# Performance work log

Hardware: AMD Instinct MI355X
Metric: run time of the kernel (lower is better)

Reference implementation:

```python
import jax, jax.numpy as jnp
import numpy as np

B, N, D, H = 4, 1024, 1024, 16
DH = D // H
SCALE = jnp.sqrt(jnp.float32(DH))


def setup_inputs() -> dict:
    key = jax.random.key(0)
    ks = jax.random.split(key, 12)
    Q = jax.random.normal(ks[0], (B, N, D), dtype=jnp.float32)
    K = jax.random.normal(ks[1], (B, N, D), dtype=jnp.float32)
    V = jax.random.normal(ks[2], (B, N, D), dtype=jnp.float32)
    mask = jax.random.bernoulli(ks[3], 0.1, (B, H, N, N))
    w_scale = 0.02
    Wq = jax.random.normal(ks[4], (D, D), dtype=jnp.float32) * w_scale
    Wk = jax.random.normal(ks[5], (D, D), dtype=jnp.float32) * w_scale
    Wv = jax.random.normal(ks[6], (D, D), dtype=jnp.float32) * w_scale
    Wo = jax.random.normal(ks[7], (D, D), dtype=jnp.float32) * w_scale
    bq = jax.random.normal(ks[8], (D,), dtype=jnp.float32) * w_scale
    bk = jax.random.normal(ks[9], (D,), dtype=jnp.float32) * w_scale
    bv = jax.random.normal(ks[10], (D,), dtype=jnp.float32) * w_scale
    bo = jax.random.normal(ks[11], (D,), dtype=jnp.float32) * w_scale
    return {"Q": Q, "K": K, "V": V, "mask": mask,
            "Wq": Wq, "bq": bq, "Wk": Wk, "bk": bk,
            "Wv": Wv, "bv": bv, "Wo": Wo, "bo": bo}


def _split_heads(x):
    # [b, n, (h d)] -> [b, h, n, d]
    b, n, _ = x.shape
    return x.reshape(b, n, H, DH).transpose(0, 2, 1, 3)


def reference(Q, K, V, mask, Wq, bq, Wk, bk, Wv, bv, Wo, bo):
    # torch nn.Linear: y = x @ W.T + b
    q = _split_heads(Q @ Wq.T + bq)
    k = _split_heads(K @ Wk.T + bk)
    v = _split_heads(V @ Wv.T + bv)
    # scores: [b, h, n, n]
    scores = jnp.einsum('bhnd,bhmd->bhnm', q, k) / SCALE
    scores = jnp.where(mask, jnp.float32(-1e10), scores)
    weights = jax.nn.softmax(scores, axis=-1)
    attn = jnp.einsum('bhnm,bhmd->bhnd', weights, v)
    x = attn.transpose(0, 2, 1, 3).reshape(Q.shape[0], Q.shape[1], D)
    x = x @ Wo.T + bo
    return (x, weights)
```

## Files before the change

### kernel.cpp

```cpp
#include <hip/hip_runtime.h>


#define SEQ   1024
#define D_DIM 1024
#define HEADS 16
#define DHEAD 64
#define BATCH 4

typedef __attribute__((ext_vector_type(8))) short bhalf8;
typedef __attribute__((ext_vector_type(4))) float floatx4;

typedef __attribute__((address_space(1))) const void GlobCV;
typedef __attribute__((address_space(3))) void LdsV;

static __device__ __forceinline__ unsigned short f2b(float f) {
    unsigned int u = __float_as_uint(f);
    u += 0x7FFFu + ((u >> 16) & 1u);
    return (unsigned short)(u >> 16);
}

static __device__ __forceinline__ void gload16(const void* g, void* l) {
    __builtin_amdgcn_global_load_lds((GlobCV*)g, (LdsV*)l, 16, 0, 0);
}

__global__ __launch_bounds__(256) void detect_mask_kernel(const uint4* __restrict__ m,
                                                          int* __restrict__ flag) {
    __shared__ int found;
    if (threadIdx.x == 0) found = 0;
    __syncthreads();
    unsigned int bad = 0;
#pragma unroll
    for (int i = 0; i < 16; ++i) {
        uint4 w = m[threadIdx.x + i * 256];
        unsigned int a = w.x, b = w.y, c = w.z, d = w.w;
        bad |= (a != 0u && a != 1u && a != 0x3F800000u);
        bad |= (b != 0u && b != 1u && b != 0x3F800000u);
        bad |= (c != 0u && c != 1u && c != 0x3F800000u);
        bad |= (d != 0u && d != 1u && d != 0x3F800000u);
    }
    if (bad) atomicOr(&found, 1);
    __syncthreads();
    if (threadIdx.x == 0) *flag = found;
}

__global__ __launch_bounds__(256) void mask_pack(const void* __restrict__ mask,
                                                 const int* __restrict__ mflagp,
                                                 unsigned int* __restrict__ bits) {
    const size_t idx = (size_t)blockIdx.x * 256 + threadIdx.x;
    unsigned int w = 0;
    if (*mflagp) {
        const uint4* p = (const uint4*)mask + idx * 2;
        uint4 a = p[0], b = p[1];
        unsigned int d[8] = {a.x, a.y, a.z, a.w, b.x, b.y, b.z, b.w};
#pragma unroll
        for (int i = 0; i < 8; ++i) {
            unsigned int x = d[i];
            w |= (((x & 0x000000FFu) != 0u) ? 1u : 0u) << (i * 4 + 0);
            w |= (((x & 0x0000FF00u) != 0u) ? 1u : 0u) << (i * 4 + 1);
            w |= (((x & 0x00FF0000u) != 0u) ? 1u : 0u) << (i * 4 + 2);
            w |= (((x & 0xFF000000u) != 0u) ? 1u : 0u) << (i * 4 + 3);
        }
    } else {
        const uint4* p = (const uint4*)mask + idx * 8;
#pragma unroll
        for (int i = 0; i < 8; ++i) {
            uint4 a = p[i];
            w |= (a.x ? 1u : 0u) << (i * 4 + 0);
            w |= (a.y ? 1u : 0u) << (i * 4 + 1);
            w |= (a.z ? 1u : 0u) << (i * 4 + 2);
            w |= (a.w ? 1u : 0u) << (i * 4 + 3);
        }
    }
    bits[idx] = w;
}

__global__ __launch_bounds__(256) void cast_f2b_all(const float* __restrict__ Q,
                                                    const float* __restrict__ K,
                                                    const float* __restrict__ V,
                                                    const float* __restrict__ Wq,
                                                    const float* __restrict__ Wk,
                                                    const float* __restrict__ Wv,
                                                    const float* __restrict__ Wo,
                                                    unsigned short* __restrict__ Ab,
                                                    unsigned short* __restrict__ Wb) {
    const int y = blockIdx.y;
    const float* src;
    unsigned short* dst;
    int nblocks;
    if (y < 3) {
        src = (y == 0) ? Q : (y == 1) ? K : V;
        dst = Ab + ((size_t)y << 22);
        nblocks = 2048;
    } else {
        src = (y == 3) ? Wq : (y == 4) ? Wk : (y == 5) ? Wv : Wo;
        dst = Wb + ((size_t)(y - 3) << 20);
        nblocks = 512;
    }
    if (blockIdx.x >= (unsigned)nblocks) return;
    const size_t i = ((size_t)blockIdx.x * 256 + threadIdx.x) * 8;
    float4 f0 = *(const float4*)&src[i];
    float4 f1 = *(const float4*)&src[i + 4];
    ushort4 h0, h1;
    h0.x = f2b(f0.x); h0.y = f2b(f0.y); h0.z = f2b(f0.z); h0.w = f2b(f0.w);
    h1.x = f2b(f1.x); h1.y = f2b(f1.y); h1.z = f2b(f1.z); h1.w = f2b(f1.w);
    *(ushort4*)&dst[i] = h0;
    *(ushort4*)&dst[i + 4] = h1;
}

template <int OMODE>
__global__ __launch_bounds__(256) void gemm_lds(const unsigned short* __restrict__ Abase,
                                                const unsigned short* __restrict__ Wbase,
                                                const float* __restrict__ b0,
                                                const float* __restrict__ b1,
                                                const float* __restrict__ b2,
                                                void* __restrict__ Obase) {
    __shared__ unsigned short Al[128 * 64];
    __shared__ unsigned short Bl[128 * 64];

    const int tid = threadIdx.x;
    const int lane = tid & 63, wid = tid >> 6;
    const int lr = lane & 15, lq = lane >> 4;
    const int wm = (wid & 1) * 64, wn = (wid >> 1) * 64;
    const int rowBase = blockIdx.y * 128;
    const int colBase = blockIdx.x * 128;
    const int z = blockIdx.z;

    const unsigned short* A = Abase + ((size_t)z << 22);
    const unsigned short* W = Wbase + ((size_t)z << 20);
    const float* bias = (z == 0) ? b0 : (z == 1) ? b1 : b2;

    const int srow = lane >> 3;
    const int scol = (lane & 7) * 8;

    floatx4 acc[4][4];
#pragma unroll
    for (int mi = 0; mi < 4; ++mi)
#pragma unroll
        for (int ni = 0; ni < 4; ++ni)
#pragma unroll
            for (int r = 0; r < 4; ++r) acc[mi][ni][r] = 0.f;

    for (int k0 = 0; k0 < D_DIM; k0 += 64) {
#pragma unroll
        for (int i = 0; i < 4; ++i) {
            int chunk = wid * 4 + i;
            gload16(&A[(size_t)(rowBase + chunk * 8 + srow) * D_DIM + k0 + scol],
                    &Al[chunk * 512]);
        }
#pragma unroll
        for (int i = 0; i < 4; ++i) {
            int chunk = wid * 4 + i;
            gload16(&W[(size_t)(colBase + chunk * 8 + srow) * D_DIM + k0 + scol],
                    &Bl[chunk * 512]);
        }
        __syncthreads();
#pragma unroll
        for (int ks = 0; ks < 2; ++ks) {
            bhalf8 af[4], bfr[4];
#pragma unroll
            for (int mi = 0; mi < 4; ++mi)
                af[mi] = *(const bhalf8*)&Al[(wm + mi * 16 + lr) * 64 + ks * 32 + lq * 8];
#pragma unroll
            for (int ni = 0; ni < 4; ++ni)
                bfr[ni] = *(const bhalf8*)&Bl[(wn + ni * 16 + lr) * 64 + ks * 32 + lq * 8];
#pragma unroll
            for (int mi = 0; mi < 4; ++mi)
#pragma unroll
                for (int ni = 0; ni < 4; ++ni)
                    acc[mi][ni] = __builtin_amdgcn_mfma_f32_16x16x32_bf16(af[mi], bfr[ni],
                                                                          acc[mi][ni], 0, 0, 0);
        }
        __syncthreads();
    }

#pragma unroll
    for (int mi = 0; mi < 4; ++mi) {
#pragma unroll
        for (int ni = 0; ni < 4; ++ni) {
            int col = colBase + wn + ni * 16 + lr;
            float bv = bias[col];
#pragma unroll
            for (int r = 0; r < 4; ++r) {
                int m = rowBase + wm + mi * 16 + lq * 4 + r;
                float v = acc[mi][ni][r] + bv;
                if (OMODE == 0) {
                    unsigned short* o = (unsigned short*)Obase + ((size_t)z << 22);
                    int b = m >> 10, n = m & 1023, h = col >> 6, dh = col & 63;
                    o[(((size_t)(b * HEADS + h)) << 16) + (n << 6) + dh] = f2b(v);
                } else {
                    float* o = (float*)Obase;
                    o[(size_t)m * D_DIM + col] = v;
                }
            }
        }
    }
}

__global__ __launch_bounds__(256, 4) void attn_kernel(const unsigned short* __restrict__ qh,
                                                      const unsigned short* __restrict__ kh,
                                                      const unsigned short* __restrict__ vh,
                                                      const unsigned int* __restrict__ bits,
                                                      float* __restrict__ wout,
                                                      unsigned short* __restrict__ attnb) {
    __shared__ unsigned short ql[64 * 64];
    __shared__ unsigned short kl[64 * 64];
    __shared__ unsigned short vtl[64 * 64];
    __shared__ unsigned short pl[64 * 64];
    __shared__ unsigned int maskw[64 * 32];

    const int tid = threadIdx.x;
    const int lane = tid & 63, wid = tid >> 6;
    const int lr = lane & 15, lq = lane >> 4;

    const int wg = blockIdx.x;
    const int xcd = wg & 7, tt = wg >> 3;
    const int bh = ((tt >> 4) << 3) | xcd;
    const int row0 = (tt & 15) << 6;

    const size_t hoff = (size_t)bh << 16;
    const unsigned short* qp = qh + hoff;
    const unsigned short* kp = kh + hoff;
    const unsigned short* vp = vh + hoff;

#pragma unroll
    for (int i = 0; i < 2; ++i) {
        int id = tid + i * 256;
        int r = id >> 3, c8 = id & 7;
        *(uint4*)&ql[r * 64 + ((c8 ^ (r & 7)) << 3)] =
            *(const uint4*)&qp[((size_t)(row0 + r) << 6) + c8 * 8];
    }
    {
        const unsigned int* src = bits + ((size_t)bh * SEQ + row0) * 32;
#pragma unroll
        for (int i = 0; i < 2; ++i) {
            int id = tid + i * 256;
            *(uint4*)&maskw[id * 4] = *(const uint4*)&src[id * 4];
        }
    }

    uint4 kreg0, kreg1, vreg0, vreg1;
#define LOADK(j)                                                                          \
    {                                                                                     \
        kreg0 = *(const uint4*)&kp[((size_t)(((j) << 6) + (tid >> 3)) << 6) + (tid & 7) * 8];        \
        kreg1 = *(const uint4*)&kp[((size_t)(((j) << 6) + ((tid + 256) >> 3)) << 6) + (tid & 7) * 8]; \
    }
#define STOREK                                                                  \
    {                                                                           \
        int r0 = tid >> 3, c0 = tid & 7, r1 = (tid + 256) >> 3;                 \
        *(uint4*)&kl[r0 * 64 + ((c0 ^ (r0 & 7)) << 3)] = kreg0;                 \
        *(uint4*)&kl[r1 * 64 + ((c0 ^ (r1 & 7)) << 3)] = kreg1;                 \
    }
#define LOADV(j)                                                                          \
    {                                                                                     \
        vreg0 = *(const uint4*)&vp[((size_t)(((j) << 6) + (tid & 63)) << 6) + ((tid >> 6) * 8)];      \
        vreg1 = *(const uint4*)&vp[((size_t)(((j) << 6) + (tid & 63)) << 6) + ((tid >> 6) * 8 + 32)]; \
    }
#define STOREV                                                                  \
    {                                                                           \
        int n0 = tid & 63, d0 = (tid >> 6) * 8, d1 = d0 + 32;                   \
        const unsigned short* e0 = (const unsigned short*)&vreg0;               \
        const unsigned short* e1 = (const unsigned short*)&vreg1;               \
        _Pragma("unroll") for (int t = 0; t < 8; ++t) {                         \
            vtl[(d0 + t) * 64 + (n0 ^ (t << 3))] = e0[t];                       \
            vtl[(d1 + t) * 64 + (n0 ^ (t << 3))] = e1[t];                       \
        }                                                                       \
    }

    float m_l[4], l_l[4];
#pragma unroll
    for (int r = 0; r < 4; ++r) { m_l[r] = -3e38f; l_l[r] = 0.f; }

    LOADK(0);
    for (int j = 0; j < 16; ++j) {
        __syncthreads();
        STOREK;
        if (j < 15) LOADK(j + 1);
        __syncthreads();

        floatx4 sacc[4];
#pragma unroll
        for (int c = 0; c < 4; ++c)
#pragma unroll
            for (int r = 0; r < 4; ++r) sacc[c][r] = 0.f;
#pragma unroll
        for (int ks = 0; ks < 2; ++ks) {
            int arow = wid * 16 + lr;
            bhalf8 a = *(const bhalf8*)&ql[arow * 64 + (((ks * 4 + lq) ^ (lr & 7)) << 3)];
#pragma unroll
            for (int c = 0; c < 4; ++c) {
                int brow = c * 16 + lr;
                bhalf8 bb = *(const bhalf8*)&kl[brow * 64 + (((ks * 4 + lq) ^ (lr & 7)) << 3)];
                sacc[c] = __builtin_amdgcn_mfma_f32_16x16x32_bf16(a, bb, sacc[c], 0, 0, 0);
            }
        }
        unsigned int w0[4], w1[4];
#pragma unroll
        for (int r = 0; r < 4; ++r) {
            int row = wid * 16 + lq * 4 + r;
            w0[r] = maskw[row * 32 + j * 2];
            w1[r] = maskw[row * 32 + j * 2 + 1];
        }
#pragma unroll
        for (int c = 0; c < 4; ++c) {
            int sh = lr + ((c & 1) << 4);
#pragma unroll
            for (int r = 0; r < 4; ++r) {
                unsigned int w = (c >> 1) ? w1[r] : w0[r];
                float s = sacc[c][r] * 0.125f;
                sacc[c][r] = ((w >> sh) & 1u) ? -1e10f : s;
            }
        }
#pragma unroll
        for (int r = 0; r < 4; ++r) {
            float mx = fmaxf(fmaxf(sacc[0][r], sacc[1][r]), fmaxf(sacc[2][r], sacc[3][r]));
            float mn = fmaxf(m_l[r], mx);
            float sv = __expf(sacc[0][r] - mn) + __expf(sacc[1][r] - mn) +
                       __expf(sacc[2][r] - mn) + __expf(sacc[3][r] - mn);
            l_l[r] = l_l[r] * __expf(m_l[r] - mn) + sv;
            m_l[r] = mn;
        }
    }
#pragma unroll
    for (int o = 1; o < 16; o <<= 1) {
#pragma unroll
        for (int r = 0; r < 4; ++r) {
            float mo = __shfl_xor(m_l[r], o);
            float lo = __shfl_xor(l_l[r], o);
            float mn = fmaxf(m_l[r], mo);
            l_l[r] = l_l[r] * __expf(m_l[r] - mn) + lo * __expf(mo - mn);
            m_l[r] = mn;
        }
    }
    float invl[4];
#pragma unroll
    for (int r = 0; r < 4; ++r) invl[r] = 1.f / l_l[r];

    floatx4 oacc[4];
#pragma unroll
    for (int c = 0; c < 4; ++c)
#pragma unroll
        for (int r = 0; r < 4; ++r) oacc[c][r] = 0.f;
    const size_t wrowbase = ((size_t)bh * SEQ + row0) * SEQ;

    LOADK(0);
    LOADV(0);
    for (int j = 0; j < 16; ++j) {
        __syncthreads();
        STOREK;
        STOREV;
        if (j < 15) { LOADK(j + 1); LOADV(j + 1); }
        __syncthreads();

        floatx4 sacc[4];
#pragma unroll
        for (int c = 0; c < 4; ++c)
#pragma unroll
            for (int r = 0; r < 4; ++r) sacc[c][r] = 0.f;
#pragma unroll
        for (int ks = 0; ks < 2; ++ks) {
            int arow = wid * 16 + lr;
            bhalf8 a = *(const bhalf8*)&ql[arow * 64 + (((ks * 4 + lq) ^ (lr & 7)) << 3)];
#pragma unroll
            for (int c = 0; c < 4; ++c) {
                int brow = c * 16 + lr;
                bhalf8 bb = *(const bhalf8*)&kl[brow * 64 + (((ks * 4 + lq) ^ (lr & 7)) << 3)];
                sacc[c] = __builtin_amdgcn_mfma_f32_16x16x32_bf16(a, bb, sacc[c], 0, 0, 0);
            }
        }
        unsigned int w0[4], w1[4];
#pragma unroll
        for (int r = 0; r < 4; ++r) {
            int row = wid * 16 + lq * 4 + r;
            w0[r] = maskw[row * 32 + j * 2];
            w1[r] = maskw[row * 32 + j * 2 + 1];
        }
#pragma unroll
        for (int c = 0; c < 4; ++c) {
            int sh = lr + ((c & 1) << 4);
            int col = (j << 6) + c * 16 + lr;
#pragma unroll
            for (int r = 0; r < 4; ++r) {
                unsigned int w = (c >> 1) ? w1[r] : w0[r];
                int row = wid * 16 + lq * 4 + r;
                float s = sacc[c][r] * 0.125f;
                if ((w >> sh) & 1u) s = -1e10f;
                float p = __expf(s - m_l[r]) * invl[r];
                wout[wrowbase + (size_t)row * SEQ + col] = p;
                pl[row * 64 + ((c * 16 + lr) ^ ((row & 7) << 3))] = f2b(p);
            }
        }
#pragma unroll
        for (int ks = 0; ks < 2; ++ks) {
            int arow = wid * 16 + lr;
            bhalf8 a = *(const bhalf8*)&pl[arow * 64 + (((ks * 4 + lq) ^ (lr & 7)) << 3)];
#pragma unroll
            for (int c = 0; c < 4; ++c) {
                int brow = c * 16 + lr;
                bhalf8 bb = *(const bhalf8*)&vtl[brow * 64 + (((ks * 4 + lq) ^ (lr & 7)) << 3)];
                oacc[c] = __builtin_amdgcn_mfma_f32_16x16x32_bf16(a, bb, oacc[c], 0, 0, 0);
            }
        }
    }

    const int b = bh >> 4, h = bh & 15;
#pragma unroll
    for (int c = 0; c < 4; ++c) {
        int colg = h * 64 + c * 16 + lr;
#pragma unroll
        for (int r = 0; r < 4; ++r) {
            int n = row0 + wid * 16 + lq * 4 + r;
            attnb[(size_t)(b * SEQ + n) * D_DIM + colg] = f2b(oacc[c][r]);
        }
    }
#undef LOADK
#undef STOREK
#undef LOADV
#undef STOREV
}

extern "C" void kernel_launch(void* const* d_in, const int* in_sizes, int n_in,
                              void* d_out, int out_size, void* d_ws, size_t ws_size,
                              hipStream_t stream) {
    const float* Q = (const float*)d_in[0];
    const float* K = (const float*)d_in[1];
    const float* V = (const float*)d_in[2];
    const void* mask = d_in[3];
    const float* Wq = (const float*)d_in[4];
    const float* bq = (const float*)d_in[5];
    const float* Wk = (const float*)d_in[6];
    const float* bk = (const float*)d_in[7];
    const float* Wv = (const float*)d_in[8];
    const float* bv = (const float*)d_in[9];
    const float* Wo = (const float*)d_in[10];
    const float* bo = (const float*)d_in[11];

    char* ws = (char*)d_ws;
    int* mflag = (int*)ws;
    unsigned short* qhb = (unsigned short*)(ws + 256);
    unsigned short* khb = qhb + 4194304;
    unsigned short* vhb = khb + 4194304;
    unsigned short* attnb = vhb + 4194304;
    unsigned int* bitsbuf = (unsigned int*)(attnb + 4194304);
    unsigned short* Wbf = (unsigned short*)(bitsbuf + 2097152);

    unsigned short* Abf =
        (unsigned short*)((char*)d_out + (size_t)out_size - (size_t)3 * 4194304 * 2);

    float* xout = (float*)d_out;
    float* wout = xout + (size_t)BATCH * SEQ * D_DIM;

    dim3 blk(256);
    detect_mask_kernel<<<1, blk, 0, stream>>>((const uint4*)mask, mflag);
    mask_pack<<<dim3(8192), blk, 0, stream>>>(mask, mflag, bitsbuf);
    cast_f2b_all<<<dim3(2048, 7), blk, 0, stream>>>(Q, K, V, Wq, Wk, Wv, Wo, Abf, Wbf);

    gemm_lds<0><<<dim3(8, 32, 3), blk, 0, stream>>>(Abf, Wbf, bq, bk, bv, qhb);

    attn_kernel<<<dim3(1024), blk, 0, stream>>>(qhb, khb, vhb, bitsbuf, wout, attnb);

    gemm_lds<1><<<dim3(8, 32, 1), blk, 0, stream>>>(attnb, Wbf + 3 * 1048576, bo, bo, bo, xout);
}
```

Measured before the change: 645.8 us.

## Double-buffer GEMM LDS tiles with swizzle and use nontemporal output stores

The projection GEMM now uses two half-depth (K=32) LDS buffers, so the next tile's global-to-LDS loads are issued before computing on the current one, with a single barrier per step. It also XOR-swizzles the LDS layout to reduce bank conflicts on fragment reads. Output stores for the fp32 GEMM result and the large attention-weights matrix become nontemporal to avoid polluting cache. The risk is that the prefetched loads are not awaited before the barrier in a way that guarantees completion, and halving the K depth per step doubles the number of barriers.

Result: no change. 656.9 us (+1.7%).

```diff
diff --git a/kernel.cpp b/kernel.cpp
--- a/kernel.cpp
+++ b/kernel.cpp
@@ -114,8 +114,8 @@
                                                 const float* __restrict__ b1,
                                                 const float* __restrict__ b2,
                                                 void* __restrict__ Obase) {
-    __shared__ unsigned short Al[128 * 64];
-    __shared__ unsigned short Bl[128 * 64];
+    __shared__ unsigned short Al[2][128 * 32];
+    __shared__ unsigned short Bl[2][128 * 32];
 
     const int tid = threadIdx.x;
     const int lane = tid & 63, wid = tid >> 6;
@@ -129,8 +129,39 @@
     const unsigned short* W = Wbase + ((size_t)z << 20);
     const float* bias = (z == 0) ? b0 : (z == 1) ? b1 : b2;
 
-    const int srow = lane >> 3;
-    const int scol = (lane & 7) * 8;
+    const int srow = lane >> 2;
+    const int scol = ((lane & 3) ^ (srow & 3)) * 8;
+
+#define STAGE(buf, k0)                                                              \
+    {                                                                               \
+        _Pragma("unroll") for (int i = 0; i < 2; ++i) {                             \
+            int chunk = wid * 2 + i;                                                \
+            gload16(&A[(size_t)(rowBase + chunk * 16 + srow) * D_DIM + (k0) + scol],\
+                    &Al[buf][chunk * 512]);                                         \
+        }                                                                           \
+        _Pragma("unroll") for (int i = 0; i < 2; ++i) {                             \
+            int chunk = wid * 2 + i;                                                \
+            gload16(&W[(size_t)(colBase + chunk * 16 + srow) * D_DIM + (k0) + scol],\
+                    &Bl[buf][chunk * 512]);                                         \
+        }                                                                           \
+    }
+
+#define COMPUTE(buf)                                                                \
+    {                                                                               \
+        bhalf8 af[4], bfr[4];                                                       \
+        _Pragma("unroll") for (int mi = 0; mi < 4; ++mi) {                          \
+            int row = wm + mi * 16 + lr;                                            \
+            af[mi] = *(const bhalf8*)&Al[buf][row * 32 + ((lq ^ (row & 3)) << 3)];  \
+        }                                                                           \
+        _Pragma("unroll") for (int ni = 0; ni < 4; ++ni) {                          \
+            int row = wn + ni * 16 + lr;                                            \
+            bfr[ni] = *(const bhalf8*)&Bl[buf][row * 32 + ((lq ^ (row & 3)) << 3)]; \
+        }                                                                           \
+        _Pragma("unroll") for (int mi = 0; mi < 4; ++mi)                            \
+            _Pragma("unroll") for (int ni = 0; ni < 4; ++ni)                        \
+                acc[mi][ni] = __builtin_amdgcn_mfma_f32_16x16x32_bf16(              \
+                    af[mi], bfr[ni], acc[mi][ni], 0, 0, 0);                         \
+    }
 
     floatx4 acc[4][4];
 #pragma unroll
@@ -140,38 +171,17 @@
 #pragma unroll
             for (int r = 0; r < 4; ++r) acc[mi][ni][r] = 0.f;
 
-    for (int k0 = 0; k0 < D_DIM; k0 += 64) {
-#pragma unroll
-        for (int i = 0; i < 4; ++i) {
-            int chunk = wid * 4 + i;
-            gload16(&A[(size_t)(rowBase + chunk * 8 + srow) * D_DIM + k0 + scol],
-                    &Al[chunk * 512]);
-        }
-#pragma unroll
-        for (int i = 0; i < 4; ++i) {
-            int chunk = wid * 4 + i;
-            gload16(&W[(size_t)(colBase + chunk * 8 + srow) * D_DIM + k0 + scol],
-                    &Bl[chunk * 512]);
-        }
+    STAGE(0, 0);
+    __syncthreads();
+    for (int t = 0; t < 31; ++t) {
+        STAGE((t + 1) & 1, (t + 1) << 5);
+        COMPUTE(t & 1);
         __syncthreads();
-#pragma unroll
-        for (int ks = 0; ks < 2; ++ks) {
-            bhalf8 af[4], bfr[4];
-#pragma unroll
-            for (int mi = 0; mi < 4; ++mi)
-                af[mi] = *(const bhalf8*)&Al[(wm + mi * 16 + lr) * 64 + ks * 32 + lq * 8];
-#pragma unroll
-            for (int ni = 0; ni < 4; ++ni)
-                bfr[ni] = *(const bhalf8*)&Bl[(wn + ni * 16 + lr) * 64 + ks * 32 + lq * 8];
-#pragma unroll
-            for (int mi = 0; mi < 4; ++mi)
-#pragma unroll
-                for (int ni = 0; ni < 4; ++ni)
-                    acc[mi][ni] = __builtin_amdgcn_mfma_f32_16x16x32_bf16(af[mi], bfr[ni],
-                                                                          acc[mi][ni], 0, 0, 0);
-        }
-        __syncthreads();
-    }
+    }
+    COMPUTE(1);
+
+#undef STAGE
+#undef COMPUTE
 
 #pragma unroll
     for (int mi = 0; mi < 4; ++mi) {
@@ -189,7 +199,7 @@
                     o[(((size_t)(b * HEADS + h)) << 16) + (n << 6) + dh] = f2b(v);
                 } else {
                     float* o = (float*)Obase;
-                    o[(size_t)m * D_DIM + col] = v;
+                    __builtin_nontemporal_store(v, &o[(size_t)m * D_DIM + col]);
                 }
             }
         }
@@ -385,7 +395,7 @@
                 float s = sacc[c][r] * 0.125f;
                 if ((w >> sh) & 1u) s = -1e10f;
                 float p = __expf(s - m_l[r]) * invl[r];
-                wout[wrowbase + (size_t)row * SEQ + col] = p;
+                __builtin_nontemporal_store(p, &wout[wrowbase + (size_t)row * SEQ + col]);
                 pl[row * 64 + ((c * 16 + lr) ^ ((row & 7) << 3))] = f2b(p);
             }
         }
```
